# Optimization experiments

Measured on AMD Instinct MI355X. Metric: run time of the kernel, lower is better.

## Reference

```python
import jax, jax.numpy as jnp
import numpy as np
from jax import lax

FILTER_SIZE = 11
SIGMA = 1.5
K1, K2 = 0.01, 0.03
WEIGHTS = jnp.array([0.0448, 0.2856, 0.3001, 0.2363, 0.1333], dtype=jnp.float32)


def _gauss_1d(size, sigma):
    coords = jnp.arange(size, dtype=jnp.float32) - (size - 1) / 2.0
    return jax.nn.softmax(-coords ** 2 / (2.0 * sigma ** 2))


def _gaussian_filter(x, k1d):
    # separable depthwise blur, VALID padding: horizontal then vertical
    C = x.shape[1]
    size = k1d.shape[0]
    kw = jnp.broadcast_to(k1d.reshape(1, 1, 1, size), (C, 1, 1, size))  # OIHW
    kh = jnp.broadcast_to(k1d.reshape(1, 1, size, 1), (C, 1, size, 1))
    dn = ('NCHW', 'OIHW', 'NCHW')
    x = lax.conv_general_dilated(x, kw, (1, 1), 'VALID', dimension_numbers=dn, feature_group_count=C)
    x = lax.conv_general_dilated(x, kh, (1, 1), 'VALID', dimension_numbers=dn, feature_group_count=C)
    return x


def _ssim(x, y, k1d, max_val):
    c1 = (K1 * max_val) ** 2
    c2 = (K2 * max_val) ** 2
    mu1 = _gaussian_filter(x, k1d)
    mu2 = _gaussian_filter(y, k1d)
    mu1_sq, mu2_sq, mu1_mu2 = mu1 ** 2, mu2 ** 2, mu1 * mu2
    sigma1_sq = _gaussian_filter(x * x, k1d) - mu1_sq
    sigma2_sq = _gaussian_filter(y * y, k1d) - mu2_sq
    sigma12 = _gaussian_filter(x * y, k1d) - mu1_mu2
    cs_map = (2 * sigma12 + c2) / (sigma1_sq + sigma2_sq + c2)
    ssim_map = (2 * mu1_mu2 + c1) / (mu1_sq + mu2_sq + c1) * cs_map
    return ssim_map.mean(axis=(-1, -2, -3)), cs_map.mean(axis=(-1, -2, -3))


def _avg_pool2(x):
    # torch avg_pool2d(kernel=2, padding=(H%2, W%2)), count_include_pad=True
    ph, pw = x.shape[-2] % 2, x.shape[-1] % 2
    if ph or pw:
        x = jnp.pad(x, ((0, 0), (0, 0), (ph, ph), (pw, pw)))
    N, C, H, W = x.shape
    return x.reshape(N, C, H // 2, 2, W // 2, 2).mean(axis=(-3, -1))


def setup_inputs() -> dict:
    key = jax.random.key(0)
    k1, k2 = jax.random.split(key)
    shape = (32, 3, 512, 512)
    return {
        'input': jax.random.uniform(k1, shape, dtype=jnp.float32),
        'target': jax.random.uniform(k2, shape, dtype=jnp.float32),
    }


def reference(input, target):
    k1d = _gauss_1d(FILTER_SIZE, SIGMA)
    max_val = target.max() - target.min()  # module default: max_val=None
    levels = WEIGHTS.shape[0]
    x, y = input, target
    mcs = []
    ssim_val = None
    for _ in range(levels):
        ssim_val, cs = _ssim(x, y, k1d, max_val)
        mcs.append(cs)
        x = _avg_pool2(x)
        y = _avg_pool2(y)
    mcs = jnp.stack(mcs, axis=0)  # (levels, N)
    # faithful to original: ssim_val ** w[-1] broadcast inside the product
    ms = jnp.prod(mcs[:-1] ** WEIGHTS[:-1, None] * ssim_val ** WEIGHTS[-1], axis=0)
    return ms.mean()
```

## Files before the change

### kernel.cpp

```cpp
#include <hip/hip_runtime.h>
#include <cmath>

#define FILT 11

typedef float v2f __attribute__((ext_vector_type(2)));

struct GW { float w[FILT]; };

__device__ __forceinline__ unsigned enc_f(float f) {
    unsigned u = __float_as_uint(f);
    return (u & 0x80000000u) ? ~u : (u | 0x80000000u);
}
__device__ __forceinline__ float dec_f(unsigned u) {
    return (u & 0x80000000u) ? __uint_as_float(u & 0x7FFFFFFFu)
                             : __uint_as_float(~u);
}

__global__ void init_acc(unsigned* ws) {
    int t = threadIdx.x;
    if (t == 0) { ws[0] = 0u; ws[1] = 0xFFFFFFFFu; }
    for (int i = 2 + t; i < 512; i += blockDim.x) ws[i] = 0u;
}

__global__ void minmax_kernel(const float4* __restrict__ t, long n4, unsigned* mm) {
    unsigned mx = 0u, mn = 0xFFFFFFFFu;
    long stride = (long)gridDim.x * blockDim.x;
    for (long i = (long)blockIdx.x * blockDim.x + threadIdx.x; i < n4; i += stride) {
        float4 v = t[i];
        unsigned a = enc_f(v.x), b = enc_f(v.y), c = enc_f(v.z), d = enc_f(v.w);
        mx = max(mx, max(max(a, b), max(c, d)));
        mn = min(mn, min(min(a, b), min(c, d)));
    }
    for (int off = 32; off; off >>= 1) {
        mx = max(mx, (unsigned)__shfl_down((int)mx, off));
        mn = min(mn, (unsigned)__shfl_down((int)mn, off));
    }
    __shared__ unsigned smx[4], smn[4];
    int wid = threadIdx.x >> 6, lane = threadIdx.x & 63;
    if (lane == 0) { smx[wid] = mx; smn[wid] = mn; }
    __syncthreads();
    if (threadIdx.x == 0) {
        for (int i = 1; i < 4; i++) { mx = max(mx, smx[i]); mn = min(mn, smn[i]); }
        atomicMax(&mm[0], mx);
        atomicMin(&mm[1], mn);
    }
}

__global__ __launch_bounds__(256) void ssim_stream(
    const float* __restrict__ x, const float* __restrict__ y,
    int H, int W, int NC, int nstrips, int nb, int B,
    const unsigned* __restrict__ mm,
    float* __restrict__ cs_sum, float* __restrict__ ssim_sum, GW gw,
    float* __restrict__ poolx, float* __restrict__ pooly, int do_pool)
{
    __shared__ v2f ring[4][2][80];

    const int wv = threadIdx.x >> 6;
    const int lane = threadIdx.x & 63;
    const int wid = blockIdx.x * 4 + wv;
    const int total = NC * nstrips * nb;
    if (wid >= total) return;

    const int band = wid % nb;
    const int t1 = wid / nb;
    const int strip = t1 % nstrips;
    const int img = t1 / nstrips;
    const int n = img / 3;

    const int Ho = H - (FILT - 1);
    const int Wo = W - (FILT - 1);
    const int out_lo = band * B;
    const int out_hi = min(out_lo + B, Ho);
    if (out_lo >= Ho) return;
    const int a = out_lo, b = out_hi + (FILT - 1);

    const int base = strip * 64;
    const float* xp = x + (size_t)img * H * W;
    const float* yp = y + (size_t)img * H * W;
    const int c0 = min(base + lane, W - 1);
    const int c1 = min(base + 64 + lane, W - 1);
    const bool colv = (base + lane) < Wo;

    const float mv = dec_f(mm[0]) - dec_f(mm[1]);
    const float c1c = (0.01f * mv) * (0.01f * mv);
    const float c2c = (0.03f * mv) * (0.03f * mv);

    const int Wp = W >> 1;
    const size_t pbase = (size_t)img * (H >> 1) * Wp;

    v2f acc01[FILT], acc23[FILT];
    float acc4[FILT];
#pragma unroll
    for (int s = 0; s < FILT; s++) {
        acc01[s] = (v2f){0.f, 0.f};
        acc23[s] = (v2f){0.f, 0.f};
        acc4[s] = 0.f;
    }

    float lcs = 0.f, lss = 0.f;

    const float* xr = xp + (size_t)a * W;
    const float* yr = yp + (size_t)a * W;
    float pfx0 = xr[c0], pfy0 = yr[c0];
    float pfx1 = xr[c1], pfy1 = yr[c1];
    xr += W; yr += W;

#pragma unroll 1
    for (int r0 = a; r0 < b; r0 += FILT) {
#pragma unroll
        for (int p = 0; p < FILT; p++) {
            const int r = r0 + p;
            if (r < b) {
                const int cur = r & 1;

                ring[wv][cur][lane] = (v2f){pfx0, pfy0};
                if (lane < 10) {
                    ring[wv][cur][64 + lane] = (v2f){pfx1, pfy1};
                }

                if (r + 1 < b) {
                    pfx0 = xr[c0]; pfy0 = yr[c0];
                    pfx1 = xr[c1]; pfy1 = yr[c1];
                    xr += W; yr += W;
                }

                __asm__ volatile("s_waitcnt lgkmcnt(0)" ::: "memory");

                v2f h01 = (v2f){0.f, 0.f};
                v2f h23 = (v2f){0.f, 0.f};
                float h4 = 0.f;
#pragma unroll
                for (int k = 0; k < FILT; k++) {
                    v2f v = ring[wv][cur][lane + k];
                    float w = gw.w[k];
                    v2f w2 = {w, w};
                    h01 = __builtin_elementwise_fma(w2, v, h01);
                    v2f sq = v * v;
                    h23 = __builtin_elementwise_fma(w2, sq, h23);
                    h4 = __builtin_fmaf(w, v.x * v.y, h4);
                }

#pragma unroll
                for (int k = 0; k < FILT; k++) {
                    const int s = (p - k + FILT) % FILT;
                    float w = gw.w[k];
                    v2f w2 = {w, w};
                    acc01[s] = __builtin_elementwise_fma(w2, h01, acc01[s]);
                    acc23[s] = __builtin_elementwise_fma(w2, h23, acc23[s]);
                    acc4[s] = __builtin_fmaf(w, h4, acc4[s]);
                }

                const int e = (p + 1) % FILT;
                if (r >= a + (FILT - 1) && colv) {
                    float m1 = acc01[e].x, m2 = acc01[e].y;
                    float mu11 = m1 * m1, mu22 = m2 * m2, mu12 = m1 * m2;
                    float s1 = acc23[e].x - mu11;
                    float s2 = acc23[e].y - mu22;
                    float s12 = acc4[e] - mu12;
                    float A = 2.f * s12 + c2c, Bv = s1 + s2 + c2c;
                    float Cv = 2.f * mu12 + c1c, Dv = mu11 + mu22 + c1c;
                    float r_ = __builtin_amdgcn_rcpf(Bv * Dv);
                    float AD = A * Dv;
                    lcs += AD * r_;
                    lss += Cv * A * r_;
                }
                acc01[e] = (v2f){0.f, 0.f};
                acc23[e] = (v2f){0.f, 0.f};
                acc4[e] = 0.f;

                if (do_pool && (r & 1) && r > a && lane < 32) {
                    const int pc = (base >> 1) + lane;
                    if (pc < Wp) {
                        v2f q00 = ring[wv][cur ^ 1][2 * lane];
                        v2f q01 = ring[wv][cur ^ 1][2 * lane + 1];
                        v2f q10 = ring[wv][cur][2 * lane];
                        v2f q11 = ring[wv][cur][2 * lane + 1];
                        v2f s = (q00 + q01 + q10 + q11) * (v2f){0.25f, 0.25f};
                        size_t o = pbase + (size_t)(r >> 1) * Wp + pc;
                        poolx[o] = s.x;
                        pooly[o] = s.y;
                    }
                }
            }
        }
    }

    for (int off = 32; off; off >>= 1) {
        lcs += __shfl_down(lcs, off);
        lss += __shfl_down(lss, off);
    }
    if (lane == 0) {
        atomicAdd(&cs_sum[n], lcs);
        atomicAdd(&ssim_sum[n], lss);
    }
}

__global__ void final_kernel(const float* __restrict__ cs_sum,
                             const float* __restrict__ ssim_sum,
                             float* __restrict__ out)
{
    const float cnt[5] = {3.f * 502 * 502, 3.f * 246 * 246, 3.f * 118 * 118,
                          3.f * 54 * 54, 3.f * 22 * 22};
    const float wts[5] = {0.0448f, 0.2856f, 0.3001f, 0.2363f, 0.1333f};
    int n = threadIdx.x;
    float ms = 0.f;
    if (n < 32) {
        float ssim = ssim_sum[4 * 32 + n] / cnt[4];
        float t = powf(ssim, wts[4]);
        ms = 1.f;
        for (int l = 0; l < 4; l++) {
            float cs = cs_sum[l * 32 + n] / cnt[l];
            ms *= powf(cs, wts[l]) * t;
        }
    }
    for (int off = 32; off; off >>= 1) ms += __shfl_down(ms, off);
    if (threadIdx.x == 0) out[0] = ms / 32.f;
}

extern "C" void kernel_launch(void* const* d_in, const int* in_sizes, int n_in,
                              void* d_out, int out_size, void* d_ws, size_t ws_size,
                              hipStream_t stream) {
    const float* x0 = (const float*)d_in[0];
    const float* y0 = (const float*)d_in[1];
    float* out = (float*)d_out;
    float* ws = (float*)d_ws;
    unsigned* mm = (unsigned*)d_ws;
    float* cs_sum = ws + 2;
    float* ssim_sum = ws + 2 + 5 * 32;

    const int N = 32, C = 3, NC = N * C;
    const int Hs[5] = {512, 256, 128, 64, 32};
    const int NBs[5] = {8, 8, 10, 6, 3};

    float* wp = ws + 512;
    float* pxw[5] = {nullptr, nullptr, nullptr, nullptr, nullptr};
    float* pyw[5] = {nullptr, nullptr, nullptr, nullptr, nullptr};
    for (int l = 1; l < 5; l++) {
        size_t sz = (size_t)NC * Hs[l] * Hs[l];
        pxw[l] = wp; wp += sz;
        pyw[l] = wp; wp += sz;
    }
    const float* px[5] = {x0, pxw[1], pxw[2], pxw[3], pxw[4]};
    const float* py[5] = {y0, pyw[1], pyw[2], pyw[3], pyw[4]};

    GW gw;
    {
        double tmp[FILT], s = 0.0;
        for (int k = 0; k < FILT; k++) {
            double c = (double)k - (FILT - 1) / 2.0;
            tmp[k] = exp(-c * c / (2.0 * 1.5 * 1.5));
            s += tmp[k];
        }
        for (int k = 0; k < FILT; k++) gw.w[k] = (float)(tmp[k] / s);
    }

    init_acc<<<1, 256, 0, stream>>>(mm);
    long n4 = (long)NC * 512 * 512 / 4;
    minmax_kernel<<<2048, 256, 0, stream>>>((const float4*)y0, n4, mm);

    for (int l = 0; l < 5; l++) {
        int H = Hs[l];
        int Ho = H - (FILT - 1);
        int nstrips = (Ho + 63) / 64;
        int nb = NBs[l];
        int B = (Ho + nb - 1) / nb;
        nb = (Ho + B - 1) / B;
        int total_waves = NC * nstrips * nb;
        int grid = (total_waves + 3) / 4;
        int do_pool = (l < 4) ? 1 : 0;
        ssim_stream<<<grid, 256, 0, stream>>>(
            px[l], py[l], H, H, NC, nstrips, nb, B, mm,
            cs_sum + l * 32, ssim_sum + l * 32, gw,
            do_pool ? pxw[l + 1] : nullptr,
            do_pool ? pyw[l + 1] : nullptr, do_pool);
    }
    final_kernel<<<1, 64, 0, stream>>>(cs_sum, ssim_sum, out);
}
```

Baseline: 334.0 us.

## Deepen row prefetch to two rows and drop per-row LDS wait

Restructures the per-row pipeline so the next row is written into the alternate LDS ring slot while global loads run two rows ahead in odd/even register pairs, and removes the explicit lgkmcnt wait. The pool step is moved ahead of the next-row write so it reads the previous row before that slot is overwritten. Level-0 and level-1 block split counts are also lowered. The aim is to hide global load latency and LDS stalls, at the cost of more registers and less parallelism on the large levels.

Result: slower. 366.6 us (+9.8%).

```diff
diff --git a/kernel.cpp b/kernel.cpp
--- a/kernel.cpp
+++ b/kernel.cpp
@@ -99,11 +99,30 @@
 
     float lcs = 0.f, lss = 0.f;
 
-    const float* xr = xp + (size_t)a * W;
-    const float* yr = yp + (size_t)a * W;
-    float pfx0 = xr[c0], pfy0 = yr[c0];
-    float pfx1 = xr[c1], pfy1 = yr[c1];
-    xr += W; yr += W;
+    float ox0, oy0, ox1, oy1;
+    float ex0, ey0, ex1, ey1;
+    {
+        const float* xr0 = xp + (size_t)a * W;
+        const float* yr0 = yp + (size_t)a * W;
+        float t0 = xr0[c0], t1 = yr0[c0];
+        float t2 = xr0[c1], t3 = yr0[c1];
+        v2f* buf0 = &ring[wv][a & 1][0];
+        buf0[lane] = (v2f){t0, t1};
+        if (lane < 10) buf0[64 + lane] = (v2f){t2, t3};
+        const float* xr1 = xr0 + W;
+        const float* yr1 = yr0 + W;
+        const float* xr2 = xr0 + 2 * (size_t)W;
+        const float* yr2 = yr0 + 2 * (size_t)W;
+        if ((a + 1) & 1) {
+            ox0 = xr1[c0]; oy0 = yr1[c0]; ox1 = xr1[c1]; oy1 = yr1[c1];
+            ex0 = xr2[c0]; ey0 = yr2[c0]; ex1 = xr2[c1]; ey1 = yr2[c1];
+        } else {
+            ex0 = xr1[c0]; ey0 = yr1[c0]; ex1 = xr1[c1]; ey1 = yr1[c1];
+            ox0 = xr2[c0]; oy0 = yr2[c0]; ox1 = xr2[c1]; oy1 = yr2[c1];
+        }
+    }
+    const float* xr = xp + (size_t)min(a + 3, b - 1) * W;
+    const float* yr = yp + (size_t)min(a + 3, b - 1) * W;
 
 #pragma unroll 1
     for (int r0 = a; r0 < b; r0 += FILT) {
@@ -112,26 +131,46 @@
             const int r = r0 + p;
             if (r < b) {
                 const int cur = r & 1;
-
-                ring[wv][cur][lane] = (v2f){pfx0, pfy0};
-                if (lane < 10) {
-                    ring[wv][cur][64 + lane] = (v2f){pfx1, pfy1};
-                }
-
-                if (r + 1 < b) {
-                    pfx0 = xr[c0]; pfy0 = yr[c0];
-                    pfx1 = xr[c1]; pfy1 = yr[c1];
-                    xr += W; yr += W;
-                }
-
-                __asm__ volatile("s_waitcnt lgkmcnt(0)" ::: "memory");
+                v2f* bufc = &ring[wv][cur][0];
+                v2f* bufn = &ring[wv][cur ^ 1][0];
+
+                if (do_pool && (r & 1) && r > a && lane < 32) {
+                    const int pc = (base >> 1) + lane;
+                    if (pc < Wp) {
+                        v2f q00 = bufn[2 * lane];
+                        v2f q01 = bufn[2 * lane + 1];
+                        v2f q10 = bufc[2 * lane];
+                        v2f q11 = bufc[2 * lane + 1];
+                        v2f sm = (q00 + q01 + q10 + q11) * (v2f){0.25f, 0.25f};
+                        size_t o = pbase + (size_t)(r >> 1) * Wp + pc;
+                        poolx[o] = sm.x;
+                        pooly[o] = sm.y;
+                    }
+                }
+
+                if ((r + 1) & 1) {
+                    if (r + 1 < b) {
+                        bufn[lane] = (v2f){ox0, oy0};
+                        if (lane < 10) bufn[64 + lane] = (v2f){ox1, oy1};
+                    }
+                    ox0 = xr[c0]; oy0 = yr[c0];
+                    ox1 = xr[c1]; oy1 = yr[c1];
+                } else {
+                    if (r + 1 < b) {
+                        bufn[lane] = (v2f){ex0, ey0};
+                        if (lane < 10) bufn[64 + lane] = (v2f){ex1, ey1};
+                    }
+                    ex0 = xr[c0]; ey0 = yr[c0];
+                    ex1 = xr[c1]; ey1 = yr[c1];
+                }
+                if (r + 4 < b) { xr += W; yr += W; }
 
                 v2f h01 = (v2f){0.f, 0.f};
                 v2f h23 = (v2f){0.f, 0.f};
                 float h4 = 0.f;
 #pragma unroll
                 for (int k = 0; k < FILT; k++) {
-                    v2f v = ring[wv][cur][lane + k];
+                    v2f v = bufc[lane + k];
                     float w = gw.w[k];
                     v2f w2 = {w, w};
                     h01 = __builtin_elementwise_fma(w2, v, h01);
@@ -160,27 +199,12 @@
                     float A = 2.f * s12 + c2c, Bv = s1 + s2 + c2c;
                     float Cv = 2.f * mu12 + c1c, Dv = mu11 + mu22 + c1c;
                     float r_ = __builtin_amdgcn_rcpf(Bv * Dv);
-                    float AD = A * Dv;
-                    lcs += AD * r_;
+                    lcs += A * Dv * r_;
                     lss += Cv * A * r_;
                 }
                 acc01[e] = (v2f){0.f, 0.f};
                 acc23[e] = (v2f){0.f, 0.f};
                 acc4[e] = 0.f;
-
-                if (do_pool && (r & 1) && r > a && lane < 32) {
-                    const int pc = (base >> 1) + lane;
-                    if (pc < Wp) {
-                        v2f q00 = ring[wv][cur ^ 1][2 * lane];
-                        v2f q01 = ring[wv][cur ^ 1][2 * lane + 1];
-                        v2f q10 = ring[wv][cur][2 * lane];
-                        v2f q11 = ring[wv][cur][2 * lane + 1];
-                        v2f s = (q00 + q01 + q10 + q11) * (v2f){0.25f, 0.25f};
-                        size_t o = pbase + (size_t)(r >> 1) * Wp + pc;
-                        poolx[o] = s.x;
-                        pooly[o] = s.y;
-                    }
-                }
             }
         }
     }
@@ -230,7 +254,7 @@
 
     const int N = 32, C = 3, NC = N * C;
     const int Hs[5] = {512, 256, 128, 64, 32};
-    const int NBs[5] = {8, 8, 10, 6, 3};
+    const int NBs[5] = {4, 6, 10, 6, 3};
 
     float* wp = ws + 512;
     float* pxw[5] = {nullptr, nullptr, nullptr, nullptr, nullptr};
```

## Process row pairs per iteration with separate even/odd LDS buffers

Applied to the files above, without the earlier changes.

The streaming SSIM loop now handles two input rows per step. Each row parity gets its own LDS buffer, and the loads for the next two rows are issued together, which should raise memory-level parallelism and instruction-level parallelism. The explicit LDS wait is dropped, and pooling reads both rows with vectorized float4 LDS loads. Per-level band heights are now set directly as even row counts, so pool rows stay aligned to band starts. The trade-off is more register pressure from the doubled in-flight loads, plus more code from unrolling both row bodies.

Result: no change. 329.0 us (-1.5%).

```diff
diff --git a/kernel.cpp b/kernel.cpp
--- a/kernel.cpp
+++ b/kernel.cpp
@@ -69,16 +69,16 @@
 
     const int Ho = H - (FILT - 1);
     const int Wo = W - (FILT - 1);
-    const int out_lo = band * B;
-    const int out_hi = min(out_lo + B, Ho);
-    if (out_lo >= Ho) return;
-    const int a = out_lo, b = out_hi + (FILT - 1);
+    const int a = band * B;
+    if (a >= Ho) return;
+    const int out_hi = min(a + B, Ho);
+    const int bEnd = out_hi + (FILT - 1);
 
     const int base = strip * 64;
     const float* xp = x + (size_t)img * H * W;
     const float* yp = y + (size_t)img * H * W;
     const int c0 = min(base + lane, W - 1);
-    const int c1 = min(base + 64 + lane, W - 1);
+    const int c1 = min(base + 64 + min(lane, 9), W - 1);
     const bool colv = (base + lane) < Wo;
 
     const float mv = dec_f(mm[0]) - dec_f(mm[1]);
@@ -87,6 +87,9 @@
 
     const int Wp = W >> 1;
     const size_t pbase = (size_t)img * (H >> 1) * Wp;
+
+    v2f* bufE = &ring[wv][0][0];
+    v2f* bufO = &ring[wv][1][0];
 
     v2f acc01[FILT], acc23[FILT];
     float acc4[FILT];
@@ -99,87 +102,132 @@
 
     float lcs = 0.f, lss = 0.f;
 
-    const float* xr = xp + (size_t)a * W;
-    const float* yr = yp + (size_t)a * W;
-    float pfx0 = xr[c0], pfy0 = yr[c0];
-    float pfx1 = xr[c1], pfy1 = yr[c1];
-    xr += W; yr += W;
+    float ex0, ey0, ex1, ey1, ox0, oy0, ox1, oy1;
+    {
+        const float* xe = xp + (size_t)a * W;
+        const float* ye = yp + (size_t)a * W;
+        ex0 = xe[c0]; ey0 = ye[c0]; ex1 = xe[c1]; ey1 = ye[c1];
+        ox0 = xe[W + c0]; oy0 = ye[W + c0];
+        ox1 = xe[W + c1]; oy1 = ye[W + c1];
+    }
 
 #pragma unroll 1
-    for (int r0 = a; r0 < b; r0 += FILT) {
+    for (int r0 = a; r0 < bEnd; r0 += 22) {
 #pragma unroll
         for (int p = 0; p < FILT; p++) {
-            const int r = r0 + p;
-            if (r < b) {
-                const int cur = r & 1;
-
-                ring[wv][cur][lane] = (v2f){pfx0, pfy0};
-                if (lane < 10) {
-                    ring[wv][cur][64 + lane] = (v2f){pfx1, pfy1};
-                }
-
-                if (r + 1 < b) {
-                    pfx0 = xr[c0]; pfy0 = yr[c0];
-                    pfx1 = xr[c1]; pfy1 = yr[c1];
-                    xr += W; yr += W;
-                }
-
-                __asm__ volatile("s_waitcnt lgkmcnt(0)" ::: "memory");
-
-                v2f h01 = (v2f){0.f, 0.f};
-                v2f h23 = (v2f){0.f, 0.f};
-                float h4 = 0.f;
+            const int r = r0 + 2 * p;
+            if (r < bEnd) {
+                const bool hasO = (r + 1 < bEnd);
+                const int pe = (2 * p) % FILT;
+                const int po = (2 * p + 1) % FILT;
+
+                bufE[lane] = (v2f){ex0, ey0};
+                if (lane < 10) bufE[64 + lane] = (v2f){ex1, ey1};
+                if (hasO) {
+                    bufO[lane] = (v2f){ox0, oy0};
+                    if (lane < 10) bufO[64 + lane] = (v2f){ox1, oy1};
+                }
+
+                {
+                    const int re = min(r + 2, bEnd - 1);
+                    const int ro = min(r + 3, bEnd - 1);
+                    const float* xe = xp + (size_t)re * W;
+                    const float* ye = yp + (size_t)re * W;
+                    const float* xo = xp + (size_t)ro * W;
+                    const float* yo = yp + (size_t)ro * W;
+                    ex0 = xe[c0]; ey0 = ye[c0]; ex1 = xe[c1]; ey1 = ye[c1];
+                    ox0 = xo[c0]; oy0 = yo[c0]; ox1 = xo[c1]; oy1 = yo[c1];
+                }
+
+                if (do_pool && hasO && lane < 32) {
+                    const int pc = (base >> 1) + lane;
+                    if (pc < Wp) {
+                        float4 qe = *(const float4*)&bufE[2 * lane];
+                        float4 qo = *(const float4*)&bufO[2 * lane];
+                        size_t o = pbase + (size_t)(r >> 1) * Wp + pc;
+                        poolx[o] = 0.25f * (qe.x + qe.z + qo.x + qo.z);
+                        pooly[o] = 0.25f * (qe.y + qe.w + qo.y + qo.w);
+                    }
+                }
+
+                v2f h01e = (v2f){0.f, 0.f}, h23e = (v2f){0.f, 0.f};
+                float h4e = 0.f;
 #pragma unroll
                 for (int k = 0; k < FILT; k++) {
-                    v2f v = ring[wv][cur][lane + k];
+                    v2f v = bufE[lane + k];
                     float w = gw.w[k];
                     v2f w2 = {w, w};
-                    h01 = __builtin_elementwise_fma(w2, v, h01);
+                    h01e = __builtin_elementwise_fma(w2, v, h01e);
                     v2f sq = v * v;
-                    h23 = __builtin_elementwise_fma(w2, sq, h23);
-                    h4 = __builtin_fmaf(w, v.x * v.y, h4);
+                    h23e = __builtin_elementwise_fma(w2, sq, h23e);
+                    h4e = __builtin_fmaf(w, v.x * v.y, h4e);
                 }
 
 #pragma unroll
                 for (int k = 0; k < FILT; k++) {
-                    const int s = (p - k + FILT) % FILT;
+                    const int s = (pe - k + FILT) % FILT;
                     float w = gw.w[k];
                     v2f w2 = {w, w};
-                    acc01[s] = __builtin_elementwise_fma(w2, h01, acc01[s]);
-                    acc23[s] = __builtin_elementwise_fma(w2, h23, acc23[s]);
-                    acc4[s] = __builtin_fmaf(w, h4, acc4[s]);
-                }
-
-                const int e = (p + 1) % FILT;
+                    acc01[s] = __builtin_elementwise_fma(w2, h01e, acc01[s]);
+                    acc23[s] = __builtin_elementwise_fma(w2, h23e, acc23[s]);
+                    acc4[s] = __builtin_fmaf(w, h4e, acc4[s]);
+                }
+
+                const int eE = (pe + 1) % FILT;
                 if (r >= a + (FILT - 1) && colv) {
-                    float m1 = acc01[e].x, m2 = acc01[e].y;
+                    float m1 = acc01[eE].x, m2 = acc01[eE].y;
                     float mu11 = m1 * m1, mu22 = m2 * m2, mu12 = m1 * m2;
-                    float s1 = acc23[e].x - mu11;
-                    float s2 = acc23[e].y - mu22;
-                    float s12 = acc4[e] - mu12;
+                    float s1 = acc23[eE].x - mu11;
+                    float s2 = acc23[eE].y - mu22;
+                    float s12 = acc4[eE] - mu12;
                     float A = 2.f * s12 + c2c, Bv = s1 + s2 + c2c;
                     float Cv = 2.f * mu12 + c1c, Dv = mu11 + mu22 + c1c;
                     float r_ = __builtin_amdgcn_rcpf(Bv * Dv);
-                    float AD = A * Dv;
-                    lcs += AD * r_;
+                    lcs += A * Dv * r_;
                     lss += Cv * A * r_;
                 }
-                acc01[e] = (v2f){0.f, 0.f};
-                acc23[e] = (v2f){0.f, 0.f};
-                acc4[e] = 0.f;
-
-                if (do_pool && (r & 1) && r > a && lane < 32) {
-                    const int pc = (base >> 1) + lane;
-                    if (pc < Wp) {
-                        v2f q00 = ring[wv][cur ^ 1][2 * lane];
-                        v2f q01 = ring[wv][cur ^ 1][2 * lane + 1];
-                        v2f q10 = ring[wv][cur][2 * lane];
-                        v2f q11 = ring[wv][cur][2 * lane + 1];
-                        v2f s = (q00 + q01 + q10 + q11) * (v2f){0.25f, 0.25f};
-                        size_t o = pbase + (size_t)(r >> 1) * Wp + pc;
-                        poolx[o] = s.x;
-                        pooly[o] = s.y;
+                acc01[eE] = (v2f){0.f, 0.f};
+                acc23[eE] = (v2f){0.f, 0.f};
+                acc4[eE] = 0.f;
+
+                if (hasO) {
+                    v2f h01o = (v2f){0.f, 0.f}, h23o = (v2f){0.f, 0.f};
+                    float h4o = 0.f;
+#pragma unroll
+                    for (int k = 0; k < FILT; k++) {
+                        v2f v = bufO[lane + k];
+                        float w = gw.w[k];
+                        v2f w2 = {w, w};
+                        h01o = __builtin_elementwise_fma(w2, v, h01o);
+                        v2f sq = v * v;
+                        h23o = __builtin_elementwise_fma(w2, sq, h23o);
+                        h4o = __builtin_fmaf(w, v.x * v.y, h4o);
                     }
+#pragma unroll
+                    for (int k = 0; k < FILT; k++) {
+                        const int s = (po - k + FILT) % FILT;
+                        float w = gw.w[k];
+                        v2f w2 = {w, w};
+                        acc01[s] = __builtin_elementwise_fma(w2, h01o, acc01[s]);
+                        acc23[s] = __builtin_elementwise_fma(w2, h23o, acc23[s]);
+                        acc4[s] = __builtin_fmaf(w, h4o, acc4[s]);
+                    }
+                    const int eO = (po + 1) % FILT;
+                    if (r >= a + (FILT - 1) && colv) {
+                        float m1 = acc01[eO].x, m2 = acc01[eO].y;
+                        float mu11 = m1 * m1, mu22 = m2 * m2, mu12 = m1 * m2;
+                        float s1 = acc23[eO].x - mu11;
+                        float s2 = acc23[eO].y - mu22;
+                        float s12 = acc4[eO] - mu12;
+                        float A = 2.f * s12 + c2c, Bv = s1 + s2 + c2c;
+                        float Cv = 2.f * mu12 + c1c, Dv = mu11 + mu22 + c1c;
+                        float r_ = __builtin_amdgcn_rcpf(Bv * Dv);
+                        lcs += A * Dv * r_;
+                        lss += Cv * A * r_;
+                    }
+                    acc01[eO] = (v2f){0.f, 0.f};
+                    acc23[eO] = (v2f){0.f, 0.f};
+                    acc4[eO] = 0.f;
                 }
             }
         }
@@ -230,7 +278,7 @@
 
     const int N = 32, C = 3, NC = N * C;
     const int Hs[5] = {512, 256, 128, 64, 32};
-    const int NBs[5] = {8, 8, 10, 6, 3};
+    const int Bs[5] = {64, 42, 12, 10, 8};
 
     float* wp = ws + 512;
     float* pxw[5] = {nullptr, nullptr, nullptr, nullptr, nullptr};
@@ -262,9 +310,8 @@
         int H = Hs[l];
         int Ho = H - (FILT - 1);
         int nstrips = (Ho + 63) / 64;
-        int nb = NBs[l];
-        int B = (Ho + nb - 1) / nb;
-        nb = (Ho + B - 1) / B;
+        int B = Bs[l];
+        int nb = (Ho + B - 1) / B;
         int total_waves = NC * nstrips * nb;
         int grid = (total_waves + 3) / 4;
         int do_pool = (l < 4) ? 1 : 0;
```
